# Performance work log

Measured on AMD Instinct MI355X. Metric: run time of the kernel, lower is better.

Reference implementation:

```python
import jax, jax.numpy as jnp
import numpy as np
import math

B, C, H, W = 8, 512, 32, 32
NUM_GROUPS = 32
NUM_HEADS = C // 64  # num_head_channels=64 -> 8 heads
EPS = 1e-5


def setup_inputs() -> dict:
    key = jax.random.key(0)
    ks = jax.random.split(key, 7)
    x = jax.random.normal(ks[0], (B, C, H, W), dtype=jnp.float32)
    gn_w = jax.random.uniform(ks[1], (C,), dtype=jnp.float32, minval=0.5, maxval=1.5)
    gn_b = jax.random.normal(ks[2], (C,), dtype=jnp.float32) * 0.1
    qkv_w = jax.random.normal(ks[3], (3 * C, C), dtype=jnp.float32) * 0.02
    qkv_b = jax.random.normal(ks[4], (3 * C,), dtype=jnp.float32) * 0.02
    proj_w = jax.random.normal(ks[5], (C, C), dtype=jnp.float32) * 0.02
    proj_b = jax.random.normal(ks[6], (C,), dtype=jnp.float32) * 0.02
    return {"x": x, "gn_w": gn_w, "gn_b": gn_b, "qkv_w": qkv_w,
            "qkv_b": qkv_b, "proj_w": proj_w, "proj_b": proj_b}


def _group_norm(x, w, b):
    # x: [B, C, L]
    bb, cc, ll = x.shape
    g = x.reshape(bb, NUM_GROUPS, cc // NUM_GROUPS, ll)
    mean = g.mean(axis=(2, 3), keepdims=True)
    var = g.var(axis=(2, 3), keepdims=True)
    g = (g - mean) * jax.lax.rsqrt(var + EPS)
    return g.reshape(bb, cc, ll) * w[None, :, None] + b[None, :, None]


def reference(x, gn_w, gn_b, qkv_w, qkv_b, proj_w, proj_b):
    b, c, h, w = x.shape
    L = h * w
    xf = x.reshape(b, c, L)
    # 1x1 conv1d QKV on normalized input: weight [3C, C]
    qkv = jnp.einsum('oc,bcl->bol', qkv_w, _group_norm(xf, gn_w, gn_b)) + qkv_b[None, :, None]
    ch = c // NUM_HEADS  # per-head channels
    qkv = qkv.reshape(b * NUM_HEADS, 3 * ch, L)
    q, k, v = qkv[:, :ch], qkv[:, ch:2 * ch], qkv[:, 2 * ch:]
    scale = 1.0 / math.sqrt(math.sqrt(ch))
    # [b*H, T, S] scores, softmax over source dim (computed in fp32 per source)
    weight = jnp.einsum('bct,bcs->bts', q * scale, k * scale)
    weight = jax.nn.softmax(weight.astype(jnp.float32), axis=-1).astype(weight.dtype)
    a = jnp.einsum('bts,bcs->bct', weight, v).reshape(b, c, L)
    hproj = jnp.einsum('oc,bcl->bol', proj_w, a) + proj_b[None, :, None]
    return (xf + hproj).reshape(b, c, h, w)
```

## Files before the change

### kernel.cpp

```cpp
#include <hip/hip_runtime.h>
#include <math.h>

#define BB 8
#define CC 512
#define LL 1024
#define GG 32
#define CPG 16
#define NH 8
#define CH 64

typedef unsigned short ushort_t;
typedef __attribute__((ext_vector_type(8))) short short8;
typedef __attribute__((ext_vector_type(4))) float f32x4;

#define SCALE_Q 0.18033688f

__device__ inline ushort_t f2bf(float f) {
  union { float f; unsigned u; } v;
  v.f = f;
  unsigned r = v.u + 0x7FFFu + ((v.u >> 16) & 1u);
  return (ushort_t)(r >> 16);
}

__device__ inline unsigned pack_bf2(float lo, float hi) {
  return __builtin_amdgcn_perm(__float_as_uint(hi), __float_as_uint(lo),
                               0x07060302u);
}

__device__ inline int swz(int r, int k) {
  return r * 64 + ((((k >> 3) ^ (r & 7)) << 3) | (k & 7));
}

__global__ __launch_bounds__(256) void gn_stats_kernel(
    const float* __restrict__ x, const float* __restrict__ gn_w,
    const float* __restrict__ gn_b, float* __restrict__ s_bc,
    float* __restrict__ t_bc) {
  int b = blockIdx.x / GG;
  int g = blockIdx.x % GG;
  const float* xg = x + ((size_t)b * CC + (size_t)g * CPG) * LL;
  float sum = 0.f, sq = 0.f;
  for (int i = threadIdx.x; i < CPG * LL; i += 256) {
    float v = xg[i];
    sum += v;
    sq += v * v;
  }
#pragma unroll
  for (int off = 32; off > 0; off >>= 1) {
    sum += __shfl_down(sum, off);
    sq += __shfl_down(sq, off);
  }
  __shared__ float red[8];
  __shared__ float st[2];
  int wave = threadIdx.x >> 6;
  if ((threadIdx.x & 63) == 0) {
    red[wave] = sum;
    red[4 + wave] = sq;
  }
  __syncthreads();
  if (threadIdx.x == 0) {
    float s = red[0] + red[1] + red[2] + red[3];
    float q = red[4] + red[5] + red[6] + red[7];
    float mean = s * (1.f / (CPG * LL));
    float var = q * (1.f / (CPG * LL)) - mean * mean;
    st[0] = mean;
    st[1] = rsqrtf(var + 1e-5f);
  }
  __syncthreads();
  if (threadIdx.x < CPG) {
    int c = g * CPG + threadIdx.x;
    float w = gn_w[c];
    float sc = st[1] * w;
    s_bc[b * CC + c] = sc;
    t_bc[b * CC + c] = gn_b[c] - st[0] * sc;
  }
}

__global__ __launch_bounds__(256) void convert_w_kernel(
    const float* __restrict__ qkv_w, const float* __restrict__ proj_w,
    ushort_t* __restrict__ wq, ushort_t* __restrict__ wp) {
  int idx = (blockIdx.x * 256 + threadIdx.x) * 4;
  const int N1 = 3 * CC * CC;
  float4 v;
  ushort_t* dst;
  if (idx < N1) {
    v = *(const float4*)(qkv_w + idx);
    dst = wq + idx;
  } else {
    int j = idx - N1;
    v = *(const float4*)(proj_w + j);
    dst = wp + j;
  }
  unsigned lo = f2bf(v.x) | ((unsigned)f2bf(v.y) << 16);
  unsigned hi = f2bf(v.z) | ((unsigned)f2bf(v.w) << 16);
  *(uint2*)dst = make_uint2(lo, hi);
}

__global__ __launch_bounds__(256) void xnt_kernel(
    const float* __restrict__ x, const float* __restrict__ s_bc,
    const float* __restrict__ t_bc, ushort_t* __restrict__ xnT) {
  const int b = blockIdx.z;
  const int c0 = blockIdx.y * 64;
  const int l0 = blockIdx.x * 64;
  const int tid = threadIdx.x;
  __shared__ ushort_t Ts[64 * 72];
#pragma unroll
  for (int r4 = 0; r4 < 4; ++r4) {
    int c_local = (tid >> 4) + r4 * 16;
    int l_local = (tid & 15) * 4;
    int c = c0 + c_local;
    float sc = s_bc[b * CC + c], sh = t_bc[b * CC + c];
    float4 v = *(const float4*)(x + ((size_t)b * CC + c) * LL + l0 + l_local);
    float vv[4] = {v.x, v.y, v.z, v.w};
#pragma unroll
    for (int dl = 0; dl < 4; ++dl) {
      int l = l_local + dl;
      int cs = c_local ^ (((l >> 2) & 7) << 3);
      Ts[l * 72 + cs] = f2bf(vv[dl] * sc + sh);
    }
  }
  __syncthreads();
#pragma unroll
  for (int rep = 0; rep < 2; ++rep) {
    int gid = tid + rep * 256;
    int l = gid >> 3, seg = gid & 7;
    uint4 v = *(const uint4*)&Ts[l * 72 + ((seg * 8) ^ (((l >> 2) & 7) << 3))];
    *(uint4*)(xnT + ((size_t)b * LL + l0 + l) * CC + c0 + seg * 8) = v;
  }
}

__global__ __launch_bounds__(256) void qkv_mfma_kernel(
    const ushort_t* __restrict__ wq, const ushort_t* __restrict__ xnT,
    const float* __restrict__ qkv_b, ushort_t* __restrict__ qT,
    ushort_t* __restrict__ kT, ushort_t* __restrict__ vbuf) {
  const int b = blockIdx.z;
  const int m0 = blockIdx.y * 128;
  const int n0 = blockIdx.x * 128;
  const int tid = threadIdx.x;
  const int w = tid >> 6, lane = tid & 63;
  const int col = lane & 15, quad = lane >> 4;
  const int wm = (w >> 1) * 64, wn = (w & 1) * 64;
  __shared__ ushort_t Smem[2 * 128 * 64];
  ushort_t* As = Smem;
  ushort_t* Bs = Smem + 128 * 64;
  f32x4 acc[4][4];
  f32x4 z = {0.f, 0.f, 0.f, 0.f};
#pragma unroll
  for (int i = 0; i < 4; ++i)
#pragma unroll
    for (int j = 0; j < 4; ++j) acc[i][j] = z;

  for (int k0 = 0; k0 < CC; k0 += 64) {
    __syncthreads();
#pragma unroll
    for (int rep = 0; rep < 4; ++rep) {
      int gid = tid + rep * 256;
      int r = gid >> 3, g = gid & 7;
      uint4 av = *(const uint4*)(wq + (size_t)(m0 + r) * CC + k0 + g * 8);
      *(uint4*)&As[swz(r, g * 8)] = av;
      uint4 bv =
          *(const uint4*)(xnT + ((size_t)b * LL + n0 + r) * CC + k0 + g * 8);
      *(uint4*)&Bs[swz(r, g * 8)] = bv;
    }
    __syncthreads();
#pragma unroll
    for (int kk = 0; kk < 2; ++kk) {
      short8 af[4], bf[4];
#pragma unroll
      for (int mi = 0; mi < 4; ++mi)
        af[mi] = *(const short8*)&As[swz(wm + mi * 16 + col, kk * 32 + quad * 8)];
#pragma unroll
      for (int ni = 0; ni < 4; ++ni)
        bf[ni] = *(const short8*)&Bs[swz(wn + ni * 16 + col, kk * 32 + quad * 8)];
#pragma unroll
      for (int mi = 0; mi < 4; ++mi)
#pragma unroll
        for (int ni = 0; ni < 4; ++ni)
          acc[mi][ni] = __builtin_amdgcn_mfma_f32_16x16x32_bf16(
              af[mi], bf[ni], acc[mi][ni], 0, 0, 0);
    }
  }
  __syncthreads();
  const int chunk_g = (m0 >> 6) + (w >> 1);
  const int sel = chunk_g % 3;
  ushort_t* Tile = Smem + (w >> 1) * 8192;
  if (sel < 2) {
    const float sc = (sel == 0) ? SCALE_Q : 1.f;
#pragma unroll
    for (int mi = 0; mi < 4; ++mi) {
      int mg = m0 + wm + mi * 16 + quad * 4;
      float b0 = qkv_b[mg + 0], b1 = qkv_b[mg + 1];
      float b2 = qkv_b[mg + 2], b3 = qkv_b[mg + 3];
      int ch = mi * 16 + quad * 4;
#pragma unroll
      for (int ni = 0; ni < 4; ++ni) {
        int lloc = wn + ni * 16 + col;
        float v0 = (acc[mi][ni][0] + b0) * sc;
        float v1 = (acc[mi][ni][1] + b1) * sc;
        float v2 = (acc[mi][ni][2] + b2) * sc;
        float v3 = (acc[mi][ni][3] + b3) * sc;
        int chs = ch ^ ((lloc & 7) << 3);
        *(uint2*)&Tile[lloc * 64 + chs] =
            make_uint2(pack_bf2(v0, v1), pack_bf2(v2, v3));
      }
    }
  } else {
#pragma unroll
    for (int mi = 0; mi < 4; ++mi)
#pragma unroll
      for (int r = 0; r < 4; ++r) {
        int ch = mi * 16 + quad * 4 + r;
        float bias = qkv_b[m0 + wm + ch];
#pragma unroll
        for (int ni = 0; ni < 4; ++ni) {
          int lloc = wn + ni * 16 + col;
          Tile[ch * 128 + lloc] =
              (ushort_t)(__float_as_uint(acc[mi][ni][r] + bias) >> 16);
        }
      }
  }
  __syncthreads();
#pragma unroll
  for (int ci = 0; ci < 2; ++ci) {
    int cg = (m0 >> 6) + ci;
    int head = cg / 3, sel2 = cg % 3;
    int bh = b * NH + head;
    ushort_t* T2 = Smem + ci * 8192;
    if (sel2 < 2) {
      ushort_t* dst = (sel2 == 0) ? qT : kT;
#pragma unroll
      for (int it = 0; it < 4; ++it) {
        int idx = tid + it * 256;
        int l = idx >> 3, seg = idx & 7;
        uint4 v = *(const uint4*)&T2[l * 64 + ((seg * 8) ^ ((l & 7) << 3))];
        *(uint4*)(dst + ((size_t)bh * LL + n0 + l) * CH + seg * 8) = v;
      }
    } else {
#pragma unroll
      for (int it = 0; it < 4; ++it) {
        int idx = tid + it * 256;
        int ch = idx >> 4, lseg = idx & 15;
        uint4 v = *(const uint4*)&T2[ch * 128 + lseg * 8];
        *(uint4*)(vbuf + ((size_t)bh * CH + ch) * LL + n0 + lseg * 8) = v;
      }
    }
  }
}

__global__ __launch_bounds__(256) void attn_mfma_kernel(
    const ushort_t* __restrict__ qT, const ushort_t* __restrict__ kT,
    const ushort_t* __restrict__ vbuf, ushort_t* __restrict__ abuf) {
  const int B = blockIdx.x;
  const int bh = (B & 7) * 8 + ((B >> 3) >> 4);
  const int t0g = ((B >> 3) & 15) * 64;
  const int b = bh >> 3, h = bh & 7;
  const int tid = threadIdx.x;
  const int w = tid >> 6, lane = tid & 63;
  const int col = lane & 15, quad = lane >> 4;
  const int strip = w * 16;
  __shared__ ushort_t QPs[64 * 64];
  __shared__ ushort_t Ks[64 * 64];
  __shared__ ushort_t Vs[64 * 64];

#pragma unroll
  for (int rep = 0; rep < 2; ++rep) {
    int gid = tid + rep * 256;
    int r = gid >> 3, g = gid & 7;
    uint4 v = *(const uint4*)(qT + ((size_t)bh * LL + t0g + r) * CH + g * 8);
    *(uint4*)&QPs[swz(r, g * 8)] = v;
  }
  __syncthreads();
  short8 bq[2];
  bq[0] = *(const short8*)&QPs[swz(strip + col, quad * 8)];
  bq[1] = *(const short8*)&QPs[swz(strip + col, 32 + quad * 8)];

  float m_s = 0.f, lsum = 0.f;
  f32x4 oacc[4];
  f32x4 z = {0.f, 0.f, 0.f, 0.f};
#pragma unroll
  for (int ci = 0; ci < 4; ++ci) oacc[ci] = z;

  for (int s0 = 0; s0 < LL; s0 += 64) {
    __syncthreads();
#pragma unroll
    for (int rep = 0; rep < 2; ++rep) {
      int gid = tid + rep * 256;
      int r = gid >> 3, g = gid & 7;
      uint4 kv = *(const uint4*)(kT + ((size_t)bh * LL + s0 + r) * CH + g * 8);
      *(uint4*)&Ks[swz(r, g * 8)] = kv;
      uint4 vv = *(const uint4*)(vbuf + ((size_t)bh * CH + r) * LL + s0 + g * 8);
      *(uint4*)&Vs[swz(r, g * 8)] = vv;
    }
    __syncthreads();
    f32x4 sacc[4];
#pragma unroll
    for (int si = 0; si < 4; ++si) sacc[si] = z;
#pragma unroll
    for (int kk = 0; kk < 2; ++kk)
#pragma unroll
      for (int si = 0; si < 4; ++si) {
        short8 ak = *(const short8*)&Ks[swz(si * 16 + col, kk * 32 + quad * 8)];
        sacc[si] = __builtin_amdgcn_mfma_f32_16x16x32_bf16(ak, bq[kk], sacc[si], 0, 0, 0);
      }
    if (s0 == 0) {
      float mx = sacc[0][0];
#pragma unroll
      for (int si = 0; si < 4; ++si)
#pragma unroll
        for (int r = 0; r < 4; ++r) mx = fmaxf(mx, sacc[si][r]);
      mx = fmaxf(mx, __shfl_xor(mx, 16));
      mx = fmaxf(mx, __shfl_xor(mx, 32));
      m_s = mx;
    }
#pragma unroll
    for (int si = 0; si < 4; ++si) {
      float p0 = __builtin_amdgcn_exp2f(sacc[si][0] - m_s);
      float p1 = __builtin_amdgcn_exp2f(sacc[si][1] - m_s);
      float p2 = __builtin_amdgcn_exp2f(sacc[si][2] - m_s);
      float p3 = __builtin_amdgcn_exp2f(sacc[si][3] - m_s);
      lsum += (p0 + p1) + (p2 + p3);
      int base = swz(strip + col, si * 16 + quad * 4);
      *(unsigned*)&QPs[base] = pack_bf2(p0, p1);
      *(unsigned*)&QPs[base + 2] = pack_bf2(p2, p3);
    }
#pragma unroll
    for (int kk = 0; kk < 2; ++kk) {
      short8 ap = *(const short8*)&QPs[swz(strip + col, kk * 32 + quad * 8)];
#pragma unroll
      for (int ci = 0; ci < 4; ++ci) {
        short8 bv = *(const short8*)&Vs[swz(ci * 16 + col, kk * 32 + quad * 8)];
        oacc[ci] = __builtin_amdgcn_mfma_f32_16x16x32_bf16(ap, bv, oacc[ci], 0, 0, 0);
      }
    }
  }
  lsum += __shfl_xor(lsum, 16);
  lsum += __shfl_xor(lsum, 32);
  float linv[4];
#pragma unroll
  for (int r = 0; r < 4; ++r)
    linv[r] = 1.f / __shfl(lsum, (lane & 48) | (quad * 4 + r), 64);
#pragma unroll
  for (int r = 0; r < 4; ++r) {
    int l = t0g + strip + quad * 4 + r;
#pragma unroll
    for (int ci = 0; ci < 4; ++ci) {
      int c = h * CH + ci * 16 + col;
      abuf[((size_t)b * LL + l) * CC + c] = f2bf(oacc[ci][r] * linv[r]);
    }
  }
}

__global__ __launch_bounds__(256) void proj_mfma_kernel(
    const ushort_t* __restrict__ wp, const ushort_t* __restrict__ abuf,
    const float* __restrict__ proj_b, const float* __restrict__ x,
    float* __restrict__ out) {
  const int b = blockIdx.z;
  const int m0 = blockIdx.y * 64;
  const int n0 = blockIdx.x * 128;
  const int tid = threadIdx.x;
  const int w = tid >> 6, lane = tid & 63;
  const int col = lane & 15, quad = lane >> 4;
  const int wm = (w >> 1) * 32, wn = (w & 1) * 64;
  __shared__ ushort_t As[64 * 64];
  __shared__ ushort_t Bs[128 * 64];
  f32x4 acc[2][4];
  f32x4 z = {0.f, 0.f, 0.f, 0.f};
#pragma unroll
  for (int i = 0; i < 2; ++i)
#pragma unroll
    for (int j = 0; j < 4; ++j) acc[i][j] = z;

  for (int k0 = 0; k0 < CC; k0 += 64) {
    __syncthreads();
#pragma unroll
    for (int rep = 0; rep < 2; ++rep) {
      int idx = tid + rep * 256;
      int r = idx >> 3, g = idx & 7;
      uint4 av = *(const uint4*)(wp + (size_t)(m0 + r) * CC + k0 + g * 8);
      *(uint4*)&As[swz(r, g * 8)] = av;
    }
#pragma unroll
    for (int rep = 0; rep < 4; ++rep) {
      int idx = tid + rep * 256;
      int r = idx >> 3, g = idx & 7;
      uint4 bv =
          *(const uint4*)(abuf + ((size_t)b * LL + n0 + r) * CC + k0 + g * 8);
      *(uint4*)&Bs[swz(r, g * 8)] = bv;
    }
    __syncthreads();
#pragma unroll
    for (int kk = 0; kk < 2; ++kk) {
      short8 af[2], bf[4];
#pragma unroll
      for (int mi = 0; mi < 2; ++mi)
        af[mi] = *(const short8*)&As[swz(wm + mi * 16 + col, kk * 32 + quad * 8)];
#pragma unroll
      for (int ni = 0; ni < 4; ++ni)
        bf[ni] = *(const short8*)&Bs[swz(wn + ni * 16 + col, kk * 32 + quad * 8)];
#pragma unroll
      for (int mi = 0; mi < 2; ++mi)
#pragma unroll
        for (int ni = 0; ni < 4; ++ni)
          acc[mi][ni] = __builtin_amdgcn_mfma_f32_16x16x32_bf16(
              af[mi], bf[ni], acc[mi][ni], 0, 0, 0);
    }
  }
#pragma unroll
  for (int mi = 0; mi < 2; ++mi)
#pragma unroll
    for (int r = 0; r < 4; ++r) {
      int o = m0 + wm + mi * 16 + quad * 4 + r;
      float bias = proj_b[o];
#pragma unroll
      for (int ni = 0; ni < 4; ++ni) {
        int l = n0 + wn + ni * 16 + col;
        size_t off = ((size_t)b * CC + o) * LL + l;
        out[off] = x[off] + bias + acc[mi][ni][r];
      }
    }
}

extern "C" void kernel_launch(void* const* d_in, const int* in_sizes, int n_in,
                              void* d_out, int out_size, void* d_ws,
                              size_t ws_size, hipStream_t stream) {
  const float* x = (const float*)d_in[0];
  const float* gn_w = (const float*)d_in[1];
  const float* gn_b = (const float*)d_in[2];
  const float* qkv_w = (const float*)d_in[3];
  const float* qkv_b = (const float*)d_in[4];
  const float* proj_w = (const float*)d_in[5];
  const float* proj_b = (const float*)d_in[6];
  float* out = (float*)d_out;

  char* ws = (char*)d_ws;
  float* s_bc = (float*)ws;
  float* t_bc = s_bc + BB * CC;
  ushort_t* wq = (ushort_t*)(t_bc + BB * CC);
  ushort_t* wp = wq + (size_t)3 * CC * CC;
  ushort_t* xnT = wp + (size_t)CC * CC;
  ushort_t* qT = xnT + (size_t)BB * LL * CC;
  ushort_t* kT = qT + (size_t)BB * NH * LL * CH;
  ushort_t* vb = kT + (size_t)BB * NH * LL * CH;
  ushort_t* abuf = vb + (size_t)BB * NH * LL * CH;

  gn_stats_kernel<<<BB * GG, 256, 0, stream>>>(x, gn_w, gn_b, s_bc, t_bc);
  convert_w_kernel<<<1024, 256, 0, stream>>>(qkv_w, proj_w, wq, wp);
  xnt_kernel<<<dim3(LL / 64, CC / 64, BB), 256, 0, stream>>>(x, s_bc, t_bc,
                                                             xnT);
  qkv_mfma_kernel<<<dim3(LL / 128, (3 * CC) / 128, BB), 256, 0, stream>>>(
      wq, xnT, qkv_b, qT, kT, vb);
  attn_mfma_kernel<<<dim3(1024), 256, 0, stream>>>(qT, kT, vb, abuf);
  proj_mfma_kernel<<<dim3(LL / 128, CC / 64, BB), 256, 0, stream>>>(
      wp, abuf, proj_b, x, out);
}
```

Before: 167.8 us.

## Process two 64-query strips per attention block to reuse K/V tiles

Each attention block now handles 128 query rows (two 64-row strips per wave) instead of 64, halving the grid to 512 blocks. Every K/V tile loaded into shared memory is used for twice as many MFMAs, which halves global K/V traffic and the barrier count per unit of work. In exchange it raises register pressure (double accumulators) and LDS use, and the smaller grid gives fewer blocks per CU on a 256-CU device.

```diff
diff --git a/kernel.cpp b/kernel.cpp
--- a/kernel.cpp
+++ b/kernel.cpp
@@ -250,34 +250,40 @@
     const ushort_t* __restrict__ qT, const ushort_t* __restrict__ kT,
     const ushort_t* __restrict__ vbuf, ushort_t* __restrict__ abuf) {
   const int B = blockIdx.x;
-  const int bh = (B & 7) * 8 + ((B >> 3) >> 4);
-  const int t0g = ((B >> 3) & 15) * 64;
+  const int bh = (B & 7) * 8 + (B >> 6);
+  const int t0g = ((B >> 3) & 7) * 128;
   const int b = bh >> 3, h = bh & 7;
   const int tid = threadIdx.x;
   const int w = tid >> 6, lane = tid & 63;
   const int col = lane & 15, quad = lane >> 4;
-  const int strip = w * 16;
-  __shared__ ushort_t QPs[64 * 64];
+  __shared__ ushort_t QPs[128 * 64];
   __shared__ ushort_t Ks[64 * 64];
   __shared__ ushort_t Vs[64 * 64];
 
 #pragma unroll
-  for (int rep = 0; rep < 2; ++rep) {
+  for (int rep = 0; rep < 4; ++rep) {
     int gid = tid + rep * 256;
     int r = gid >> 3, g = gid & 7;
     uint4 v = *(const uint4*)(qT + ((size_t)bh * LL + t0g + r) * CH + g * 8);
     *(uint4*)&QPs[swz(r, g * 8)] = v;
   }
   __syncthreads();
-  short8 bq[2];
-  bq[0] = *(const short8*)&QPs[swz(strip + col, quad * 8)];
-  bq[1] = *(const short8*)&QPs[swz(strip + col, 32 + quad * 8)];
-
-  float m_s = 0.f, lsum = 0.f;
-  f32x4 oacc[4];
+  short8 bq[2][2];
+#pragma unroll
+  for (int st = 0; st < 2; ++st)
+#pragma unroll
+    for (int kk = 0; kk < 2; ++kk)
+      bq[st][kk] =
+          *(const short8*)&QPs[swz(st * 64 + w * 16 + col, kk * 32 + quad * 8)];
+
+  float m_s[2] = {0.f, 0.f};
+  float lsum[2] = {0.f, 0.f};
+  f32x4 oacc[2][4];
   f32x4 z = {0.f, 0.f, 0.f, 0.f};
 #pragma unroll
-  for (int ci = 0; ci < 4; ++ci) oacc[ci] = z;
+  for (int st = 0; st < 2; ++st)
+#pragma unroll
+    for (int ci = 0; ci < 4; ++ci) oacc[st][ci] = z;
 
   for (int s0 = 0; s0 < LL; s0 += 64) {
     __syncthreads();
@@ -291,60 +297,81 @@
       *(uint4*)&Vs[swz(r, g * 8)] = vv;
     }
     __syncthreads();
-    f32x4 sacc[4];
-#pragma unroll
-    for (int si = 0; si < 4; ++si) sacc[si] = z;
+    f32x4 sacc[2][4];
+#pragma unroll
+    for (int st = 0; st < 2; ++st)
+#pragma unroll
+      for (int si = 0; si < 4; ++si) sacc[st][si] = z;
 #pragma unroll
     for (int kk = 0; kk < 2; ++kk)
 #pragma unroll
       for (int si = 0; si < 4; ++si) {
         short8 ak = *(const short8*)&Ks[swz(si * 16 + col, kk * 32 + quad * 8)];
-        sacc[si] = __builtin_amdgcn_mfma_f32_16x16x32_bf16(ak, bq[kk], sacc[si], 0, 0, 0);
+#pragma unroll
+        for (int st = 0; st < 2; ++st)
+          sacc[st][si] = __builtin_amdgcn_mfma_f32_16x16x32_bf16(
+              ak, bq[st][kk], sacc[st][si], 0, 0, 0);
       }
     if (s0 == 0) {
-      float mx = sacc[0][0];
-#pragma unroll
-      for (int si = 0; si < 4; ++si)
-#pragma unroll
-        for (int r = 0; r < 4; ++r) mx = fmaxf(mx, sacc[si][r]);
-      mx = fmaxf(mx, __shfl_xor(mx, 16));
-      mx = fmaxf(mx, __shfl_xor(mx, 32));
-      m_s = mx;
-    }
-#pragma unroll
-    for (int si = 0; si < 4; ++si) {
-      float p0 = __builtin_amdgcn_exp2f(sacc[si][0] - m_s);
-      float p1 = __builtin_amdgcn_exp2f(sacc[si][1] - m_s);
-      float p2 = __builtin_amdgcn_exp2f(sacc[si][2] - m_s);
-      float p3 = __builtin_amdgcn_exp2f(sacc[si][3] - m_s);
-      lsum += (p0 + p1) + (p2 + p3);
-      int base = swz(strip + col, si * 16 + quad * 4);
-      *(unsigned*)&QPs[base] = pack_bf2(p0, p1);
-      *(unsigned*)&QPs[base + 2] = pack_bf2(p2, p3);
-    }
+#pragma unroll
+      for (int st = 0; st < 2; ++st) {
+        float mx = sacc[st][0][0];
+#pragma unroll
+        for (int si = 0; si < 4; ++si)
+#pragma unroll
+          for (int r = 0; r < 4; ++r) mx = fmaxf(mx, sacc[st][si][r]);
+        mx = fmaxf(mx, __shfl_xor(mx, 16));
+        mx = fmaxf(mx, __shfl_xor(mx, 32));
+        m_s[st] = mx;
+      }
+    }
+#pragma unroll
+    for (int st = 0; st < 2; ++st)
+#pragma unroll
+      for (int si = 0; si < 4; ++si) {
+        float p0 = __builtin_amdgcn_exp2f(sacc[st][si][0] - m_s[st]);
+        float p1 = __builtin_amdgcn_exp2f(sacc[st][si][1] - m_s[st]);
+        float p2 = __builtin_amdgcn_exp2f(sacc[st][si][2] - m_s[st]);
+        float p3 = __builtin_amdgcn_exp2f(sacc[st][si][3] - m_s[st]);
+        lsum[st] += (p0 + p1) + (p2 + p3);
+        int base = swz(st * 64 + w * 16 + col, si * 16 + quad * 4);
+        *(unsigned*)&QPs[base] = pack_bf2(p0, p1);
+        *(unsigned*)&QPs[base + 2] = pack_bf2(p2, p3);
+      }
 #pragma unroll
     for (int kk = 0; kk < 2; ++kk) {
-      short8 ap = *(const short8*)&QPs[swz(strip + col, kk * 32 + quad * 8)];
+      short8 ap[2];
+#pragma unroll
+      for (int st = 0; st < 2; ++st)
+        ap[st] =
+            *(const short8*)&QPs[swz(st * 64 + w * 16 + col, kk * 32 + quad * 8)];
 #pragma unroll
       for (int ci = 0; ci < 4; ++ci) {
         short8 bv = *(const short8*)&Vs[swz(ci * 16 + col, kk * 32 + quad * 8)];
-        oacc[ci] = __builtin_amdgcn_mfma_f32_16x16x32_bf16(ap, bv, oacc[ci], 0, 0, 0);
-      }
-    }
-  }
-  lsum += __shfl_xor(lsum, 16);
-  lsum += __shfl_xor(lsum, 32);
-  float linv[4];
-#pragma unroll
-  for (int r = 0; r < 4; ++r)
-    linv[r] = 1.f / __shfl(lsum, (lane & 48) | (quad * 4 + r), 64);
-#pragma unroll
-  for (int r = 0; r < 4; ++r) {
-    int l = t0g + strip + quad * 4 + r;
-#pragma unroll
-    for (int ci = 0; ci < 4; ++ci) {
-      int c = h * CH + ci * 16 + col;
-      abuf[((size_t)b * LL + l) * CC + c] = f2bf(oacc[ci][r] * linv[r]);
+#pragma unroll
+        for (int st = 0; st < 2; ++st)
+          oacc[st][ci] = __builtin_amdgcn_mfma_f32_16x16x32_bf16(
+              ap[st], bv, oacc[st][ci], 0, 0, 0);
+      }
+    }
+  }
+#pragma unroll
+  for (int st = 0; st < 2; ++st) {
+    float ls = lsum[st];
+    ls += __shfl_xor(ls, 16);
+    ls += __shfl_xor(ls, 32);
+    float linv[4];
+#pragma unroll
+    for (int r = 0; r < 4; ++r)
+      linv[r] = 1.f / __shfl(ls, (lane & 48) | (quad * 4 + r), 64);
+#pragma unroll
+    for (int r = 0; r < 4; ++r) {
+      int l = t0g + st * 64 + w * 16 + quad * 4 + r;
+#pragma unroll
+      for (int ci = 0; ci < 4; ++ci) {
+        int c = h * CH + ci * 16 + col;
+        abuf[((size_t)b * LL + l) * CC + c] = f2bf(oacc[st][ci][r] * linv[r]);
+      }
     }
   }
 }
@@ -448,7 +475,7 @@
                                                              xnT);
   qkv_mfma_kernel<<<dim3(LL / 128, (3 * CC) / 128, BB), 256, 0, stream>>>(
       wq, xnT, qkv_b, qT, kT, vb);
-  attn_mfma_kernel<<<dim3(1024), 256, 0, stream>>>(qT, kT, vb, abuf);
+  attn_mfma_kernel<<<dim3(512), 256, 0, stream>>>(qT, kT, vb, abuf);
   proj_mfma_kernel<<<dim3(LL / 128, CC / 64, BB), 256, 0, stream>>>(
       wp, abuf, proj_b, x, out);
 }
```

After: 177.7 us. +5.9%, slower.

## Use direct global-to-LDS loads in GEMMs and merge preprocessing kernels

Applied to the files above, without the earlier changes.

The QKV and projection GEMMs now stage their tiles with global_load_lds async copies instead of register round-trips. This drops the XOR swizzle and uses a plain row-major LDS layout, which may reintroduce bank conflicts on fragment reads. The weight conversion and normalize-transpose kernels are merged into one launch to save launch overhead. The attention P tile store is merged into a single 8-byte write.

```diff
diff --git a/kernel.cpp b/kernel.cpp
--- a/kernel.cpp
+++ b/kernel.cpp
@@ -14,6 +14,13 @@
 typedef __attribute__((ext_vector_type(4))) float f32x4;
 
 #define SCALE_Q 0.18033688f
+
+typedef __attribute__((address_space(3))) unsigned as3_u32;
+typedef __attribute__((address_space(1))) unsigned as1_u32;
+
+__device__ inline void async_copy16(ushort_t* lds, const ushort_t* g) {
+  __builtin_amdgcn_global_load_lds((const as1_u32*)g, (as3_u32*)lds, 16, 0, 0);
+}
 
 __device__ inline ushort_t f2bf(float f) {
   union { float f; unsigned u; } v;
@@ -75,34 +82,36 @@
   }
 }
 
-__global__ __launch_bounds__(256) void convert_w_kernel(
+__global__ __launch_bounds__(256) void pre_kernel(
     const float* __restrict__ qkv_w, const float* __restrict__ proj_w,
-    ushort_t* __restrict__ wq, ushort_t* __restrict__ wp) {
-  int idx = (blockIdx.x * 256 + threadIdx.x) * 4;
-  const int N1 = 3 * CC * CC;
-  float4 v;
-  ushort_t* dst;
-  if (idx < N1) {
-    v = *(const float4*)(qkv_w + idx);
-    dst = wq + idx;
-  } else {
-    int j = idx - N1;
-    v = *(const float4*)(proj_w + j);
-    dst = wp + j;
-  }
-  unsigned lo = f2bf(v.x) | ((unsigned)f2bf(v.y) << 16);
-  unsigned hi = f2bf(v.z) | ((unsigned)f2bf(v.w) << 16);
-  *(uint2*)dst = make_uint2(lo, hi);
-}
-
-__global__ __launch_bounds__(256) void xnt_kernel(
+    ushort_t* __restrict__ wq, ushort_t* __restrict__ wp,
     const float* __restrict__ x, const float* __restrict__ s_bc,
     const float* __restrict__ t_bc, ushort_t* __restrict__ xnT) {
-  const int b = blockIdx.z;
-  const int c0 = blockIdx.y * 64;
-  const int l0 = blockIdx.x * 64;
+  const int Bx = blockIdx.x;
   const int tid = threadIdx.x;
   __shared__ ushort_t Ts[64 * 72];
+  if (Bx < 1024) {
+    int idx = (Bx * 256 + tid) * 4;
+    const int N1 = 3 * CC * CC;
+    float4 v;
+    ushort_t* dst;
+    if (idx < N1) {
+      v = *(const float4*)(qkv_w + idx);
+      dst = wq + idx;
+    } else {
+      int j = idx - N1;
+      v = *(const float4*)(proj_w + j);
+      dst = wp + j;
+    }
+    unsigned lo = f2bf(v.x) | ((unsigned)f2bf(v.y) << 16);
+    unsigned hi = f2bf(v.z) | ((unsigned)f2bf(v.w) << 16);
+    *(uint2*)dst = make_uint2(lo, hi);
+    return;
+  }
+  const int B2 = Bx - 1024;
+  const int b = B2 >> 7;
+  const int c0 = ((B2 >> 4) & 7) * 64;
+  const int l0 = (B2 & 15) * 64;
 #pragma unroll
   for (int r4 = 0; r4 < 4; ++r4) {
     int c_local = (tid >> 4) + r4 * 16;
@@ -155,11 +164,10 @@
     for (int rep = 0; rep < 4; ++rep) {
       int gid = tid + rep * 256;
       int r = gid >> 3, g = gid & 7;
-      uint4 av = *(const uint4*)(wq + (size_t)(m0 + r) * CC + k0 + g * 8);
-      *(uint4*)&As[swz(r, g * 8)] = av;
-      uint4 bv =
-          *(const uint4*)(xnT + ((size_t)b * LL + n0 + r) * CC + k0 + g * 8);
-      *(uint4*)&Bs[swz(r, g * 8)] = bv;
+      async_copy16(As + (size_t)(w * 64 + rep * 256) * 8,
+                   wq + (size_t)(m0 + r) * CC + k0 + g * 8);
+      async_copy16(Bs + (size_t)(w * 64 + rep * 256) * 8,
+                   xnT + ((size_t)b * LL + n0 + r) * CC + k0 + g * 8);
     }
     __syncthreads();
 #pragma unroll
@@ -167,10 +175,12 @@
       short8 af[4], bf[4];
 #pragma unroll
       for (int mi = 0; mi < 4; ++mi)
-        af[mi] = *(const short8*)&As[swz(wm + mi * 16 + col, kk * 32 + quad * 8)];
+        af[mi] =
+            *(const short8*)&As[(wm + mi * 16 + col) * 64 + kk * 32 + quad * 8];
 #pragma unroll
       for (int ni = 0; ni < 4; ++ni)
-        bf[ni] = *(const short8*)&Bs[swz(wn + ni * 16 + col, kk * 32 + quad * 8)];
+        bf[ni] =
+            *(const short8*)&Bs[(wn + ni * 16 + col) * 64 + kk * 32 + quad * 8];
 #pragma unroll
       for (int mi = 0; mi < 4; ++mi)
 #pragma unroll
@@ -299,7 +309,8 @@
 #pragma unroll
       for (int si = 0; si < 4; ++si) {
         short8 ak = *(const short8*)&Ks[swz(si * 16 + col, kk * 32 + quad * 8)];
-        sacc[si] = __builtin_amdgcn_mfma_f32_16x16x32_bf16(ak, bq[kk], sacc[si], 0, 0, 0);
+        sacc[si] =
+            __builtin_amdgcn_mfma_f32_16x16x32_bf16(ak, bq[kk], sacc[si], 0, 0, 0);
       }
     if (s0 == 0) {
       float mx = sacc[0][0];
@@ -319,8 +330,7 @@
       float p3 = __builtin_amdgcn_exp2f(sacc[si][3] - m_s);
       lsum += (p0 + p1) + (p2 + p3);
       int base = swz(strip + col, si * 16 + quad * 4);
-      *(unsigned*)&QPs[base] = pack_bf2(p0, p1);
-      *(unsigned*)&QPs[base + 2] = pack_bf2(p2, p3);
+      *(uint2*)&QPs[base] = make_uint2(pack_bf2(p0, p1), pack_bf2(p2, p3));
     }
 #pragma unroll
     for (int kk = 0; kk < 2; ++kk) {
@@ -328,7 +338,8 @@
 #pragma unroll
       for (int ci = 0; ci < 4; ++ci) {
         short8 bv = *(const short8*)&Vs[swz(ci * 16 + col, kk * 32 + quad * 8)];
-        oacc[ci] = __builtin_amdgcn_mfma_f32_16x16x32_bf16(ap, bv, oacc[ci], 0, 0, 0);
+        oacc[ci] =
+            __builtin_amdgcn_mfma_f32_16x16x32_bf16(ap, bv, oacc[ci], 0, 0, 0);
       }
     }
   }
@@ -375,16 +386,15 @@
     for (int rep = 0; rep < 2; ++rep) {
       int idx = tid + rep * 256;
       int r = idx >> 3, g = idx & 7;
-      uint4 av = *(const uint4*)(wp + (size_t)(m0 + r) * CC + k0 + g * 8);
-      *(uint4*)&As[swz(r, g * 8)] = av;
+      async_copy16(As + (size_t)(w * 64 + rep * 256) * 8,
+                   wp + (size_t)(m0 + r) * CC + k0 + g * 8);
     }
 #pragma unroll
     for (int rep = 0; rep < 4; ++rep) {
       int idx = tid + rep * 256;
       int r = idx >> 3, g = idx & 7;
-      uint4 bv =
-          *(const uint4*)(abuf + ((size_t)b * LL + n0 + r) * CC + k0 + g * 8);
-      *(uint4*)&Bs[swz(r, g * 8)] = bv;
+      async_copy16(Bs + (size_t)(w * 64 + rep * 256) * 8,
+                   abuf + ((size_t)b * LL + n0 + r) * CC + k0 + g * 8);
     }
     __syncthreads();
 #pragma unroll
@@ -392,10 +402,12 @@
       short8 af[2], bf[4];
 #pragma unroll
       for (int mi = 0; mi < 2; ++mi)
-        af[mi] = *(const short8*)&As[swz(wm + mi * 16 + col, kk * 32 + quad * 8)];
+        af[mi] =
+            *(const short8*)&As[(wm + mi * 16 + col) * 64 + kk * 32 + quad * 8];
 #pragma unroll
       for (int ni = 0; ni < 4; ++ni)
-        bf[ni] = *(const short8*)&Bs[swz(wn + ni * 16 + col, kk * 32 + quad * 8)];
+        bf[ni] =
+            *(const short8*)&Bs[(wn + ni * 16 + col) * 64 + kk * 32 + quad * 8];
 #pragma unroll
       for (int mi = 0; mi < 2; ++mi)
 #pragma unroll
@@ -443,9 +455,8 @@
   ushort_t* abuf = vb + (size_t)BB * NH * LL * CH;
 
   gn_stats_kernel<<<BB * GG, 256, 0, stream>>>(x, gn_w, gn_b, s_bc, t_bc);
-  convert_w_kernel<<<1024, 256, 0, stream>>>(qkv_w, proj_w, wq, wp);
-  xnt_kernel<<<dim3(LL / 64, CC / 64, BB), 256, 0, stream>>>(x, s_bc, t_bc,
-                                                             xnT);
+  pre_kernel<<<2048, 256, 0, stream>>>(qkv_w, proj_w, wq, wp, x, s_bc, t_bc,
+                                       xnT);
   qkv_mfma_kernel<<<dim3(LL / 128, (3 * CC) / 128, BB), 256, 0, stream>>>(
       wq, xnT, qkv_b, qT, kT, vb);
   attn_mfma_kernel<<<dim3(1024), 256, 0, stream>>>(qT, kT, vb, abuf);
```

Result: no change. 169.9 us (+1.3%).
